# Performance work log

Measured on AMD Instinct MI355X. Metric: run time of the kernel, lower is better.

The kernel has to match this reference:

```python
import jax, jax.numpy as jnp
import numpy as np

B, C, H, W = 8, 256, 80, 160   # 1/8-resolution feature maps of a 640x1280 stereo pair
DISP = 192 // 8                 # cost volume depth at 1/8 res
FACTOR = 2 ** 3                 # convex-upsample factor (n_downsample=3)
TOP_K = 3


def setup_inputs() -> dict:
    key = jax.random.key(0)
    k1, k2, k3 = jax.random.split(key, 3)
    return {
        "left": jax.random.normal(k1, (B, C, H, W), dtype=jnp.float32),
        "right": jax.random.normal(k2, (B, C, H, W), dtype=jnp.float32),
        "mask": jax.random.normal(k3, (B, 9 * FACTOR * FACTOR, H, W), dtype=jnp.float32),
        "iters": 12,
    }


def build_cost_volume(left, right):
    # cost[b,i,h,w] = mean_c left[b,c,h,w] * right[b,c,h,w-i], zero where w < i
    slices = []
    for i in range(DISP):  # fixed small structural loop over disparity shifts
        prod = jnp.mean(left[:, :, :, i:] * right[:, :, :, : W - i if i > 0 else W], axis=1)
        prod = jnp.pad(prod, ((0, 0), (0, 0), (i, 0)))
        slices.append(prod)
    return jnp.stack(slices, axis=1)  # [B, DISP, H, W]


def regression_topk(cost, k=TOP_K):
    # top-k over the disparity axis, softmax-weighted expectation of indices
    c = jnp.moveaxis(cost, 1, -1)            # [B, H, W, DISP]
    vals, inds = jax.lax.top_k(c, k)          # descending, like torch sort(1, True)[:, :k]
    w = jax.nn.softmax(vals, axis=-1)
    disp = jnp.sum(w * inds.astype(vals.dtype), axis=-1)
    return disp[:, None]                      # [B, 1, H, W]


def convex_upsample(flow, mask, iters):
    # Upsample [H,W] flow -> [8H,8W] via softmax convex combination of 3x3 neighbors.
    N, D, Hh, Ww = flow.shape
    temp = 1.0 + jnp.exp(-(jnp.float32(iters) - 1.0))  # training-mode temperature
    m = mask.reshape(N, 1, 9, FACTOR, FACTOR, Hh, Ww)
    m = jax.nn.softmax(m / temp, axis=2)
    fp = jnp.pad(FACTOR * flow, ((0, 0), (0, 0), (1, 1), (1, 1)))
    # 3x3 unfold in torch F.unfold row-major order: (dy, dx)
    patches = jnp.stack(
        [fp[:, :, dy:dy + Hh, dx:dx + Ww] for dy in range(3) for dx in range(3)], axis=2
    )  # [N, D, 9, H, W]
    up = jnp.sum(m * patches[:, :, :, None, None], axis=2)   # [N, D, F, F, H, W]
    up = up.transpose(0, 1, 4, 2, 5, 3)                      # [N, D, H, F, W, F]
    return up.reshape(N, D, FACTOR * Hh, FACTOR * Ww)


def reference(left, right, mask, iters):
    cost = build_cost_volume(left, right)
    init_disp = regression_topk(cost)                               # [B,1,H,W]
    # flow field (x-disparity channel + frozen y channel, as delta_flow[:,1]=0)
    flow = jnp.concatenate([init_disp, jnp.zeros_like(init_disp)], axis=1)
    flow_up = convex_upsample(flow, mask, iters)                    # [B,2,8H,8W]
    return -flow_up[:, :1]                                          # disparity prediction
```

## Files before the change

### kernel.cpp

```cpp
#include <hip/hip_runtime.h>
#include <cmath>

#define NBATCH 8
#define NCH    256
#define NH     80
#define NW     160
#define NDISP  24
#define FAC    8

constexpr int TPB1  = 256;
constexpr int WPB   = 4;
constexpr int NTILE = 5;
constexpr int SLOTS = 192;

typedef __attribute__((address_space(1))) unsigned int gu32;
typedef __attribute__((address_space(3))) unsigned int lu32;

__device__ __forceinline__ void gload_lds16(const float* g, float4* l) {
  __builtin_amdgcn_global_load_lds((gu32*)g, (lu32*)l, 16, 0, 0);
}

template <int N>
__device__ __forceinline__ void wait_vm() {
  if constexpr (N == 6)      asm volatile("s_waitcnt vmcnt(6)" ::: "memory");
  else if constexpr (N == 3) asm volatile("s_waitcnt vmcnt(3)" ::: "memory");
  else                       asm volatile("s_waitcnt vmcnt(0)" ::: "memory");
  __builtin_amdgcn_sched_barrier(0);
}

__device__ __forceinline__ float f4c(const float4& v, int k) {
  switch (k) { case 0: return v.x; case 1: return v.y; case 2: return v.z; default: return v.w; }
}

__global__ __launch_bounds__(TPB1) void cost_topk_kernel(
    const float* __restrict__ left, const float* __restrict__ right,
    float* __restrict__ disp)
{
  __shared__ float4 lds4[WPB][3][SLOTS];

  const int lane = threadIdx.x & 63;
  const int widx = threadIdx.x >> 6;
  const int wid  = blockIdx.x * WPB + widx;
  const int tile = wid % NTILE;
  const int row  = wid / NTILE;
  const int b    = row / NH;
  const int h    = row % NH;
  const int wb   = tile * 32;

  const int cg = lane & 7;
  const int wq = lane >> 3;

  const size_t hw = (size_t)NH * NW;
  const float* lrow = left  + (size_t)b * NCH * hw + (size_t)h * NW;
  const float* rrow = right + (size_t)b * NCH * hw + (size_t)h * NW;

  const int c0 = lane >> 4,        q0 = (lane & 15) ^ c0;
  const int c1 = 4 + (lane >> 4),  q1 = (lane & 15) ^ c1;
  const int cl = lane >> 3,        wqs = (lane & 7) ^ cl;

  int off0 = wb - 32 + 4 * q0; if (off0 < 0) off0 = 0;
  int off1 = wb - 32 + 4 * q1; if (off1 < 0) off1 = 0;

  const float* srcR0 = rrow + (size_t)(c0 * 32) * hw + off0;
  const float* srcR1 = rrow + (size_t)(c1 * 32) * hw + off1;
  const float* srcL  = lrow + (size_t)(cl * 32) * hw + wb + 4 * wqs;

#define STAGE(BUF) do {                              \
    gload_lds16(srcR0, &lds4[widx][BUF][0]);         \
    gload_lds16(srcR1, &lds4[widx][BUF][64]);        \
    gload_lds16(srcL,  &lds4[widx][BUF][128]);       \
    srcR0 += hw; srcR1 += hw; srcL += hw; } while (0)

  int rsl[7];
#pragma unroll
  for (int k = 0; k < 7; ++k) rsl[k] = cg * 16 + ((wq + 2 + k) ^ cg);
  const int lslot = 128 + cg * 8 + (wq ^ cg);

  float acc[NDISP][4];
#pragma unroll
  for (int i = 0; i < NDISP; ++i)
#pragma unroll
    for (int ws = 0; ws < 4; ++ws) acc[i][ws] = 0.f;

  auto fmastep = [&](const float4* base) {
    float4 Lq = base[lslot];
    float4 Qa = base[rsl[0]];
#pragma unroll
    for (int g = 0; g < 6; ++g) {
      float4 Qb = base[rsl[g + 1]];
      const int i0 = 20 - 4 * g;
#pragma unroll
      for (int di = 0; di < 4; ++di)
#pragma unroll
        for (int ws = 0; ws < 4; ++ws) {
          const int pos = ws - di + 4;
          float rv = (pos < 4) ? f4c(Qa, pos) : f4c(Qb, pos - 4);
          acc[i0 + di][ws] = __builtin_fmaf(f4c(Lq, ws), rv, acc[i0 + di][ws]);
        }
      Qa = Qb;
    }
  };

  const float4 fzero{0.f, 0.f, 0.f, 0.f};

#define STEP(VM, BUF, DOSTAGE) do {                                        \
    wait_vm<VM>();                                                         \
    if (tile == 0)         \
      lds4[widx][BUF][(lane >> 3) * 16 + (lane & 7)] = fzero;              \
    fmastep(&lds4[widx][BUF][0]);                                          \
    if (DOSTAGE) {                                                         \
      asm volatile("s_waitcnt lgkmcnt(0)" ::: "memory");                   \
      __builtin_amdgcn_sched_barrier(0);                                   \
      STAGE(BUF);                                                          \
    } } while (0)

  STAGE(0); STAGE(1); STAGE(2);

  for (int it = 0; it < 10; ++it) {
    STEP(6, 0, true);
    STEP(6, 1, true);
    STEP(6, 2, (it < 9));
  }
  STEP(3, 0, false);
  STEP(0, 1, false);
#undef STEP
#undef STAGE

#pragma unroll
  for (int mskm = 1; mskm < 8; mskm <<= 1)
#pragma unroll
    for (int i = 0; i < NDISP; ++i)
#pragma unroll
      for (int ws = 0; ws < 4; ++ws)
        acc[i][ws] += __shfl_xor(acc[i][ws], mskm, 64);

  if (cg == 0) {
    float o[4];
#pragma unroll
    for (int ws = 0; ws < 4; ++ws) {
      float v1 = -1e30f, v2 = -1e30f, v3 = -1e30f;
      int   j1 = 0, j2 = 0, j3 = 0;
#pragma unroll
      for (int i = 0; i < NDISP; ++i) {
        float v = acc[i][ws] * 0.00390625f;
        if (v > v1)      { v3 = v2; j3 = j2; v2 = v1; j2 = j1; v1 = v; j1 = i; }
        else if (v > v2) { v3 = v2; j3 = j2; v2 = v;  j2 = i; }
        else if (v > v3) { v3 = v;  j3 = i; }
      }
      float e2 = expf(v2 - v1), e3 = expf(v3 - v1);
      float ssum = 1.0f + e2 + e3;
      o[ws] = ((float)j1 + e2 * (float)j2 + e3 * (float)j3) / ssum;
    }
    *reinterpret_cast<float4*>(&disp[((size_t)b * NH + h) * NW + wb + wq * 4]) =
        float4{o[0], o[1], o[2], o[3]};
  }
}

__global__ __launch_bounds__(256) void upsample_kernel(
    const float* __restrict__ disp, const float* __restrict__ mask,
    const int* __restrict__ itp, float* __restrict__ out)
{
  int idx = blockIdx.x * 256 + threadIdx.x;
  const int w  = idx % NW;
  const int fy = (idx / NW) & 7;
  const int h  = (idx / (NW * FAC)) % NH;
  const int b  = idx / (NW * FAC * NH);

  const float iters = (float)itp[0];
  const float temp  = 1.0f + __expf(-(iters - 1.0f));
  const float sc    = 1.44269504088896340736f / temp;

  const size_t hw = (size_t)NH * NW;
  const float* drow = disp + (size_t)b * hw;
  float d[9];
#pragma unroll
  for (int dy = 0; dy < 3; ++dy)
#pragma unroll
    for (int dx = 0; dx < 3; ++dx) {
      int h2 = h + dy - 1, w2 = w + dx - 1;
      bool ok = (h2 >= 0) && (h2 < NH) && (w2 >= 0) && (w2 < NW);
      d[dy * 3 + dx] = ok ? drow[h2 * NW + w2] : 0.f;
    }

  const float* mb = mask + (size_t)b * 576 * hw + (size_t)h * NW + w;
  float m[9][FAC];
#pragma unroll
  for (int j = 0; j < 9; ++j)
#pragma unroll
    for (int fx = 0; fx < FAC; ++fx)
      m[j][fx] = mb[(size_t)((j * 8 + fy) * 8 + fx) * hw];

  float o[FAC];
#pragma unroll
  for (int fx = 0; fx < FAC; ++fx) {
    float mx = m[0][fx];
#pragma unroll
    for (int j = 1; j < 9; ++j) mx = fmaxf(mx, m[j][fx]);
    float ssum = 0.f, accv = 0.f;
#pragma unroll
    for (int j = 0; j < 9; ++j) {
      float e = exp2f((m[j][fx] - mx) * sc);
      ssum += e;
      accv += e * d[j];
    }
    o[fx] = (-8.0f * accv) * __builtin_amdgcn_rcpf(ssum);
  }

  float* op = out + ((size_t)b * (NH * FAC) + (size_t)(h * FAC + fy)) * (NW * FAC) + (size_t)w * FAC;
  *reinterpret_cast<float4*>(op)     = float4{o[0], o[1], o[2], o[3]};
  *reinterpret_cast<float4*>(op + 4) = float4{o[4], o[5], o[6], o[7]};
}

extern "C" void kernel_launch(void* const* d_in, const int* in_sizes, int n_in,
                              void* d_out, int out_size, void* d_ws, size_t ws_size,
                              hipStream_t stream) {
  (void)in_sizes; (void)n_in; (void)out_size; (void)ws_size;
  const float* left  = (const float*)d_in[0];
  const float* right = (const float*)d_in[1];
  const float* mask  = (const float*)d_in[2];
  const int*   iters = (const int*)d_in[3];
  float* out  = (float*)d_out;
  float* disp = (float*)d_ws;

  hipLaunchKernelGGL(cost_topk_kernel, dim3(NBATCH * NH * NTILE / WPB), dim3(TPB1), 0, stream,
                     left, right, disp);
  hipLaunchKernelGGL(upsample_kernel, dim3(NBATCH * NH * FAC * NW / 256), dim3(256), 0, stream,
                     disp, mask, iters, out);
}
```

Measured before the change: 134.4 us.

## Replace global_load_lds staging with register-staged double-buffered LDS pipeline

```diff
diff --git a/kernel.cpp b/kernel.cpp
--- a/kernel.cpp
+++ b/kernel.cpp
@@ -12,19 +12,10 @@
 constexpr int WPB   = 4;
 constexpr int NTILE = 5;
 constexpr int SLOTS = 192;
-
-typedef __attribute__((address_space(1))) unsigned int gu32;
-typedef __attribute__((address_space(3))) unsigned int lu32;
-
-__device__ __forceinline__ void gload_lds16(const float* g, float4* l) {
-  __builtin_amdgcn_global_load_lds((gu32*)g, (lu32*)l, 16, 0, 0);
-}
-
-template <int N>
-__device__ __forceinline__ void wait_vm() {
-  if constexpr (N == 6)      asm volatile("s_waitcnt vmcnt(6)" ::: "memory");
-  else if constexpr (N == 3) asm volatile("s_waitcnt vmcnt(3)" ::: "memory");
-  else                       asm volatile("s_waitcnt vmcnt(0)" ::: "memory");
+constexpr int NBUF  = 3;
+
+__device__ __forceinline__ void wait_lgkm0() {
+  asm volatile("s_waitcnt lgkmcnt(0)" ::: "memory");
   __builtin_amdgcn_sched_barrier(0);
 }
 
@@ -36,7 +27,7 @@
     const float* __restrict__ left, const float* __restrict__ right,
     float* __restrict__ disp)
 {
-  __shared__ float4 lds4[WPB][3][SLOTS];
+  __shared__ float4 lds4[WPB][NBUF][SLOTS];
 
   const int lane = threadIdx.x & 63;
   const int widx = threadIdx.x >> 6;
@@ -65,11 +56,18 @@
   const float* srcR1 = rrow + (size_t)(c1 * 32) * hw + off1;
   const float* srcL  = lrow + (size_t)(cl * 32) * hw + wb + 4 * wqs;
 
-#define STAGE(BUF) do {                              \
-    gload_lds16(srcR0, &lds4[widx][BUF][0]);         \
-    gload_lds16(srcR1, &lds4[widx][BUF][64]);        \
-    gload_lds16(srcL,  &lds4[widx][BUF][128]);       \
-    srcR0 += hw; srcR1 += hw; srcL += hw; } while (0)
+  float4* const wbase = &lds4[widx][0][0];
+
+  float4 Xr0, Xr1, Xl, Yr0, Yr1, Yl;
+
+#define LOADS(S, CH) do {                                                     \
+    S##r0 = *reinterpret_cast<const float4*>(srcR0 + (size_t)(CH) * hw);      \
+    S##r1 = *reinterpret_cast<const float4*>(srcR1 + (size_t)(CH) * hw);      \
+    S##l  = *reinterpret_cast<const float4*>(srcL  + (size_t)(CH) * hw); } while (0)
+
+#define WRITES(B, S) do {                                                     \
+    float4* bw = wbase + (B) * SLOTS;                                         \
+    bw[lane] = S##r0; bw[64 + lane] = S##r1; bw[128 + lane] = S##l; } while (0)
 
   int rsl[7];
 #pragma unroll
@@ -102,29 +100,33 @@
   };
 
   const float4 fzero{0.f, 0.f, 0.f, 0.f};
-
-#define STEP(VM, BUF, DOSTAGE) do {                                        \
-    wait_vm<VM>();                                                         \
-    if (tile == 0)         \
-      lds4[widx][BUF][(lane >> 3) * 16 + (lane & 7)] = fzero;              \
-    fmastep(&lds4[widx][BUF][0]);                                          \
-    if (DOSTAGE) {                                                         \
-      asm volatile("s_waitcnt lgkmcnt(0)" ::: "memory");                   \
-      __builtin_amdgcn_sched_barrier(0);                                   \
-      STAGE(BUF);                                                          \
-    } } while (0)
-
-  STAGE(0); STAGE(1); STAGE(2);
-
-  for (int it = 0; it < 10; ++it) {
-    STEP(6, 0, true);
-    STEP(6, 1, true);
-    STEP(6, 2, (it < 9));
+  const int azslot = (lane >> 3) * 16 + (lane & 7);
+
+  LOADS(X, 0); LOADS(Y, 1);
+  WRITES(0, X);
+  LOADS(X, 2);
+  WRITES(1, Y);
+  LOADS(Y, 3);
+
+#define STEPJ(J, S) do {                                                      \
+    wait_lgkm0();           \
+    if ((J) + 2 < 32) {                                                       \
+      WRITES(((J) + 2) % 3, S);                                               \
+      if ((J) + 4 < 32) LOADS(S, (J) + 4);                                    \
+    }                                                                         \
+    __builtin_amdgcn_sched_barrier(0);          \
+    { float4* bc = wbase + ((J) % 3) * SLOTS;                                 \
+      if (tile == 0) bc[azslot] = fzero;                                      \
+      fmastep(bc); } } while (0)
+
+#pragma unroll
+  for (int jj = 0; jj < 32; jj += 2) {
+    STEPJ(jj, X);
+    STEPJ(jj + 1, Y);
   }
-  STEP(3, 0, false);
-  STEP(0, 1, false);
-#undef STEP
-#undef STAGE
+#undef STEPJ
+#undef WRITES
+#undef LOADS
 
 #pragma unroll
   for (int mskm = 1; mskm < 8; mskm <<= 1)
```

Result: slower. 419.0 us (+211.9%).
